# Performance work log

Measured on AMD Instinct MI355X. Metric: run time of the kernel, lower is better.

## Reference

```python
import jax, jax.numpy as jnp
import numpy as np

N_CLI, N_AGG, E, D, L = 100000, 1000, 1600000, 128, 3


def setup_inputs() -> dict:
    key = jax.random.key(0)
    ks = jax.random.split(key, 16)
    inp = {
        'x_clients': jax.random.normal(ks[0], (N_CLI, D), jnp.float32),
        'x_agg': jax.random.normal(ks[1], (N_AGG, D), jnp.float32),
        'c2a_src': jax.random.randint(ks[2], (E,), 0, N_CLI, jnp.int32),
        'c2a_dst': jax.random.randint(ks[3], (E,), 0, N_AGG, jnp.int32),
        'a2c_src': jax.random.randint(ks[4], (E,), 0, N_AGG, jnp.int32),
        'a2c_dst': jax.random.randint(ks[5], (E,), 0, N_CLI, jnp.int32),
    }
    s = 1.0 / np.sqrt(D)
    # stacked per-layer SAGE params for each edge type: W_l (on aggregated msg), W_r (on dst), b
    inp['Wl_c2a'] = jax.random.uniform(ks[6], (L, D, D), jnp.float32, -s, s)
    inp['Wr_c2a'] = jax.random.uniform(ks[7], (L, D, D), jnp.float32, -s, s)
    inp['b_c2a'] = jax.random.uniform(ks[8], (L, D), jnp.float32, -s, s)
    inp['Wl_a2c'] = jax.random.uniform(ks[9], (L, D, D), jnp.float32, -s, s)
    inp['Wr_a2c'] = jax.random.uniform(ks[10], (L, D, D), jnp.float32, -s, s)
    inp['b_a2c'] = jax.random.uniform(ks[11], (L, D), jnp.float32, -s, s)
    inp['W_lin'] = jax.random.uniform(ks[12], (D, 1), jnp.float32, -s, s)
    inp['b_lin'] = jax.random.uniform(ks[13], (1,), jnp.float32, -s, s)
    return inp


def _sage(x_src, x_dst, src, dst, Wl, Wr, b, n_dst):
    # mean aggregation of gathered source features onto dst nodes
    msg = x_src[src]                                        # [E, D]
    summed = jax.ops.segment_sum(msg, dst, num_segments=n_dst)
    cnt = jax.ops.segment_sum(jnp.ones((src.shape[0], 1), x_src.dtype), dst, num_segments=n_dst)
    mean = summed / jnp.maximum(cnt, 1.0)
    return mean @ Wl + x_dst @ Wr + b


def _leaky(x):
    return jnp.where(x >= 0, x, 0.1 * x)


def reference(x_clients, x_agg, c2a_src, c2a_dst, a2c_src, a2c_dst,
              Wl_c2a, Wr_c2a, b_c2a, Wl_a2c, Wr_a2c, b_a2c, W_lin, b_lin):
    xc, xa = x_clients, x_agg
    for l in range(L):
        new_a = _sage(xc, xa, c2a_src, c2a_dst, Wl_c2a[l], Wr_c2a[l], b_c2a[l], N_AGG)
        new_c = _sage(xa, xc, a2c_src, a2c_dst, Wl_a2c[l], Wr_a2c[l], b_a2c[l], N_CLI)
        xa, xc = _leaky(new_a), _leaky(new_c)
    return (xc @ W_lin + b_lin).squeeze(1)
```

## Files before the change

### kernel.cpp

```cpp
#include <hip/hip_runtime.h>

#define D      128
#define NCLI   100000
#define NAGG   1000
#define NLAYER 3
#define NBKT   782
#define NRNG   8
#define NBIN   (NAGG * NRNG)
#define RMAGIC 343598u
#define NHIST  512
#define NCVTX  (NCLI * D / 4 / 256)
#define NCVTW  ((NLAYER * D * D + 255) / 256)
#define NROWT  (NCLI / 32)
#define CAP_E  1536

typedef short bf16x8 __attribute__((ext_vector_type(8)));
typedef float f32x16 __attribute__((ext_vector_type(16)));

static __device__ __forceinline__ float leaky(float x) { return x >= 0.f ? x : 0.1f * x; }

static __device__ __forceinline__ unsigned bf16_rn(float f) {
    unsigned u = __float_as_uint(f);
    return (u + 0x7fffu + ((u >> 16) & 1u)) >> 16;
}
static __device__ __forceinline__ float bf_val(unsigned h) { return __uint_as_float(h << 16); }
static __device__ __forceinline__ unsigned pack_bf2(float lo, float hi) {
    return bf16_rn(lo) | (bf16_rn(hi) << 16);
}
static __device__ __forceinline__ float bf_lo(unsigned v) { return __uint_as_float(v << 16); }
static __device__ __forceinline__ float bf_hi(unsigned v) { return __uint_as_float(v & 0xffff0000u); }

__global__ __launch_bounds__(256) void prep(const int* __restrict__ c2a_src,
                                            const int* __restrict__ c2a_dst,
                                            const int* __restrict__ a2c_dst, int E,
                                            int* __restrict__ cnt_ar, int* __restrict__ bcnt,
                                            const float4* __restrict__ X4,
                                            uint2* __restrict__ xhi, uint2* __restrict__ xlo,
                                            const float* __restrict__ W,
                                            unsigned short* __restrict__ Wt) {
    __shared__ int h[NBIN + NBKT];
    int bid = blockIdx.x;
    if (bid < NHIST) {
        for (int i = threadIdx.x; i < NBIN + NBKT; i += 256) h[i] = 0;
        __syncthreads();
        int stride = NHIST * 256;
        for (int e = bid * 256 + threadIdx.x; e < E; e += stride) {
            int s = c2a_src[e];
            int bin = c2a_dst[e] * NRNG + (int)__umulhi((unsigned)s, RMAGIC);
            atomicAdd(&h[bin], 1);
            atomicAdd(&h[NBIN + (a2c_dst[e] >> 7)], 1);
        }
        __syncthreads();
        for (int i = threadIdx.x; i < NBIN; i += 256)
            if (h[i]) atomicAdd(&cnt_ar[i], h[i]);
        for (int i = threadIdx.x; i < NBKT; i += 256)
            if (h[NBIN + i]) atomicAdd(&bcnt[i], h[NBIN + i]);
    } else if (bid < NHIST + NCVTX) {
        int t = (bid - NHIST) * 256 + threadIdx.x;
        float4 f = X4[t];
        unsigned h0 = bf16_rn(f.x), h1 = bf16_rn(f.y), h2 = bf16_rn(f.z), h3 = bf16_rn(f.w);
        xhi[t] = make_uint2(h0 | (h1 << 16), h2 | (h3 << 16));
        xlo[t] = make_uint2(pack_bf2(f.x - bf_val(h0), f.y - bf_val(h1)),
                            pack_bf2(f.z - bf_val(h2), f.w - bf_val(h3)));
    } else {
        int idx = (bid - NHIST - NCVTX) * 256 + threadIdx.x;
        if (idx >= NLAYER * D * D) return;
        int layer = idx >> 14, rem = idx & (D * D - 1);
        int k = rem >> 7, n = rem & 127;
        float w = W[layer * D * D + k * D + n];
        unsigned hh = bf16_rn(w);
        unsigned short* base = Wt + layer * 2 * D * D;
        base[n * D + k] = (unsigned short)hh;
        base[D * D + n * D + k] = (unsigned short)bf16_rn(w - bf_val(hh));
    }
}

__global__ void scan_both(const int* __restrict__ cnt_ar, int* __restrict__ rp_ar,
                          int* __restrict__ cur_ar, const int* __restrict__ bcnt,
                          int* __restrict__ brp, int* __restrict__ bcur) {
    __shared__ int sh[1024];
    int t = threadIdx.x;
    if (blockIdx.x == 0) {
        int v[8];
        int s = 0;
#pragma unroll
        for (int j = 0; j < 8; j++) {
            int idx = t * 8 + j;
            v[j] = (idx < NBIN) ? cnt_ar[idx] : 0;
            s += v[j];
        }
        sh[t] = s;
        __syncthreads();
        for (int off = 1; off < 1024; off <<= 1) {
            int x = (t >= off) ? sh[t - off] : 0;
            __syncthreads();
            sh[t] += x;
            __syncthreads();
        }
        int run = sh[t] - s;
#pragma unroll
        for (int j = 0; j < 8; j++) {
            int idx = t * 8 + j;
            if (idx < NBIN) {
                rp_ar[idx] = run;
                cur_ar[idx] = run;
            }
            run += v[j];
        }
        if (t == 1023) rp_ar[NBIN] = sh[1023];
    } else {
        int v = (t < NBKT) ? bcnt[t] : 0;
        sh[t] = v;
        __syncthreads();
        for (int off = 1; off < 1024; off <<= 1) {
            int x = (t >= off) ? sh[t - off] : 0;
            __syncthreads();
            sh[t] += x;
            __syncthreads();
        }
        if (t == 0) { brp[0] = 0; bcur[0] = 0; }
        if (t < NBKT) {
            brp[t + 1] = sh[t];
            if (t + 1 < NBKT) bcur[t + 1] = sh[t];
        }
    }
}

__global__ __launch_bounds__(1024) void scatter_both(const int* __restrict__ c2a_src,
                                                     const int* __restrict__ c2a_dst,
                                                     const int* __restrict__ a2c_src,
                                                     const int* __restrict__ a2c_dst, int E,
                                                     int* __restrict__ cur_ar,
                                                     int* __restrict__ col_c2a,
                                                     int* __restrict__ bcur,
                                                     int* __restrict__ sorted1) {
    __shared__ int sbuf[2 * NBIN];
    int tid = threadIdx.x;
    if (blockIdx.x < 256) {
        int* h = sbuf;
        int* base = sbuf + NBIN;
        int chunk = (E + 255) / 256;
        int e0 = blockIdx.x * chunk;
        int e1 = min(E, e0 + chunk);
        for (int i = tid; i < NBIN; i += 1024) h[i] = 0;
        __syncthreads();
        for (int e = e0 + tid; e < e1; e += 1024) {
            int s = c2a_src[e];
            atomicAdd(&h[c2a_dst[e] * NRNG + (int)__umulhi((unsigned)s, RMAGIC)], 1);
        }
        __syncthreads();
        for (int i = tid; i < NBIN; i += 1024) {
            int c = h[i];
            base[i] = c ? atomicAdd(&cur_ar[i], c) : 0;
        }
        __syncthreads();
        for (int e = e0 + tid; e < e1; e += 1024) {
            int s = c2a_src[e];
            int bin = c2a_dst[e] * NRNG + (int)__umulhi((unsigned)s, RMAGIC);
            int pos = atomicAdd(&base[bin], 1);
            col_c2a[pos] = s;
        }
    } else {
        int* h = sbuf;
        int* base = sbuf + NBKT;
        int bid = blockIdx.x - 256;
        int chunk = (E + 255) / 256;
        int e0 = bid * chunk;
        int e1 = min(E, e0 + chunk);
        for (int i = tid; i < NBKT; i += 1024) h[i] = 0;
        __syncthreads();
        for (int e = e0 + tid; e < e1; e += 1024) atomicAdd(&h[a2c_dst[e] >> 7], 1);
        __syncthreads();
        for (int i = tid; i < NBKT; i += 1024) {
            int c = h[i];
            base[i] = c ? atomicAdd(&bcur[i], c) : 0;
        }
        __syncthreads();
        for (int e = e0 + tid; e < e1; e += 1024) {
            int d = a2c_dst[e];
            int pos = atomicAdd(&base[d >> 7], 1);
            sorted1[pos] = ((d & 127) << 10) | a2c_src[e];
        }
    }
}

__global__ __launch_bounds__(512) void bucket_csr(const int* __restrict__ brp,
                                                  const int* __restrict__ sorted1,
                                                  int* __restrict__ rp_c,
                                                  int* __restrict__ col) {
    __shared__ int h[128], cur[128];
    int b = blockIdx.x, tid = threadIdx.x;
    if (tid < 128) h[tid] = 0;
    __syncthreads();
    int beg = brp[b], end = brp[b + 1];
    for (int e = beg + tid; e < end; e += 512) atomicAdd(&h[sorted1[e] >> 10], 1);
    __syncthreads();
    if (tid < 128) cur[tid] = h[tid];
    __syncthreads();
    for (int off = 1; off < 128; off <<= 1) {
        int x = 0;
        if (tid < 128 && tid >= off) x = cur[tid - off];
        __syncthreads();
        if (tid < 128) cur[tid] += x;
        __syncthreads();
    }
    if (tid < 128) {
        int start = beg + cur[tid] - h[tid];
        int c = b * 128 + tid;
        if (c < NCLI) rp_c[c] = start;
        cur[tid] = start;
    }
    if (b == NBKT - 1 && tid == 0) rp_c[NCLI] = end;
    __syncthreads();
    for (int e = beg + tid; e < end; e += 512) {
        int p = sorted1[e];
        int pos = atomicAdd(&cur[p >> 10], 1);
        col[pos] = p & 1023;
    }
}


__global__ __launch_bounds__(512) void gather_mean(const unsigned* __restrict__ tbl,
                                                   const int* __restrict__ rp_ar,
                                                   const int* __restrict__ col,
                                                   float* __restrict__ psum) {
    __shared__ float part[4][8][D];
    int quad = blockIdx.x >> 3, r = blockIdx.x & 7;
    int tid = threadIdx.x;
    int a = tid >> 7;
    int sub = (tid >> 4) & 7;
    int sl = tid & 15;
    const uint4* tbl4 = (const uint4*)tbl;
    int agg = quad * 4 + a;
    int bin = agg * NRNG + r;
    int beg = rp_ar[bin], end = rp_ar[bin + 1];
    float f0 = 0, f1 = 0, f2 = 0, f3 = 0, f4 = 0, f5 = 0, f6 = 0, f7 = 0;
    int e = beg + sub;
    for (; e + 8 < end; e += 16) {
        int s0 = col[e];
        int s1 = col[e + 8];
        uint4 v0 = tbl4[(s0 << 4) + sl];
        uint4 v1 = tbl4[(s1 << 4) + sl];
        f0 += bf_lo(v0.x); f1 += bf_hi(v0.x); f2 += bf_lo(v0.y); f3 += bf_hi(v0.y);
        f4 += bf_lo(v0.z); f5 += bf_hi(v0.z); f6 += bf_lo(v0.w); f7 += bf_hi(v0.w);
        f0 += bf_lo(v1.x); f1 += bf_hi(v1.x); f2 += bf_lo(v1.y); f3 += bf_hi(v1.y);
        f4 += bf_lo(v1.z); f5 += bf_hi(v1.z); f6 += bf_lo(v1.w); f7 += bf_hi(v1.w);
    }
    if (e < end) {
        int s0 = col[e];
        uint4 v0 = tbl4[(s0 << 4) + sl];
        f0 += bf_lo(v0.x); f1 += bf_hi(v0.x); f2 += bf_lo(v0.y); f3 += bf_hi(v0.y);
        f4 += bf_lo(v0.z); f5 += bf_hi(v0.z); f6 += bf_lo(v0.w); f7 += bf_hi(v0.w);
    }
    float* pr = &part[a][sub][sl * 8];
    pr[0] = f0; pr[1] = f1; pr[2] = f2; pr[3] = f3;
    pr[4] = f4; pr[5] = f5; pr[6] = f6; pr[7] = f7;
    __syncthreads();
    int c = tid & 127;
    float s = 0.f;
#pragma unroll
    for (int g = 0; g < 8; g++) s += part[a][g][c];
    psum[((size_t)agg * NRNG + r) * D + c] = s;
}

__global__ __launch_bounds__(128) void combine_agg(const float* __restrict__ psum,
                                                   const int* __restrict__ rp_ar,
                                                   const float* xa_old,
                                                   const float* __restrict__ Wl_a2c,
                                                   const float* __restrict__ Wl_c2a,
                                                   const float* __restrict__ Wr_c2a,
                                                   const float* __restrict__ b_c2a,
                                                   unsigned short* __restrict__ ya_bf,
                                                   float* xa_out) {
    __shared__ float mr[D], xr[D];
    int i = blockIdx.x, j = threadIdx.x;
    const float* pr = psum + (size_t)i * NRNG * D + j;
    float s = 0.f;
#pragma unroll
    for (int r = 0; r < NRNG; r++) s += pr[r * D];
    int deg = rp_ar[i * NRNG + NRNG] - rp_ar[i * NRNG];
    mr[j] = s / fmaxf((float)deg, 1.f);
    xr[j] = xa_old[i * D + j];
    __syncthreads();
    float accy = 0.f, accn = b_c2a[j];
#pragma unroll 4
    for (int k = 0; k < D; k++) {
        accy += xr[k] * Wl_a2c[k * D + j];
        accn += mr[k] * Wl_c2a[k * D + j] + xr[k] * Wr_c2a[k * D + j];
    }
    ya_bf[i * D + j] = (unsigned short)bf16_rn(accy);
    xa_out[i * D + j] = leaky(accn);
}

#define ACC8(vv) do { \
    s0 += bf_lo(vv.x); s1 += bf_hi(vv.x); s2 += bf_lo(vv.y); s3 += bf_hi(vv.y); \
    s4 += bf_lo(vv.z); s5 += bf_hi(vv.z); s6 += bf_lo(vv.w); s7 += bf_hi(vv.w); } while (0)

#define GBLOCK(SRC) do { \
    int r0 = (SRC)[0], r1 = (SRC)[1], r2 = (SRC)[2], r3 = (SRC)[3]; \
    int r4 = (SRC)[4], r5 = (SRC)[5], r6 = (SRC)[6], r7 = (SRC)[7]; \
    uint4 v0 = ya4[(r0 << 4) + q]; uint4 v1 = ya4[(r1 << 4) + q]; \
    uint4 v2 = ya4[(r2 << 4) + q]; uint4 v3 = ya4[(r3 << 4) + q]; \
    uint4 v4 = ya4[(r4 << 4) + q]; uint4 v5 = ya4[(r5 << 4) + q]; \
    uint4 v6 = ya4[(r6 << 4) + q]; uint4 v7 = ya4[(r7 << 4) + q]; \
    ACC8(v0); ACC8(v1); ACC8(v2); ACC8(v3); \
    ACC8(v4); ACC8(v5); ACC8(v6); ACC8(v7); } while (0)

#define GTAIL(SRC) do { \
    int rr = (SRC)[0]; \
    uint4 v = ya4[(rr << 4) + q]; \
    ACC8(v); } while (0)

template <int LAST>
__global__ __launch_bounds__(256) void gemm_agg(const unsigned short* __restrict__ Ahi,
                                                const unsigned short* __restrict__ Alo,
                                                const unsigned short* __restrict__ Wt,
                                                const float* __restrict__ bias,
                                                const unsigned* __restrict__ ya,
                                                const int* __restrict__ rowptr,
                                                const int* __restrict__ col,
                                                unsigned* __restrict__ xhi,
                                                unsigned* __restrict__ xlo,
                                                const float* __restrict__ Wlin,
                                                const float* __restrict__ blin,
                                                float* __restrict__ out, int E) {
    __shared__ float smem[32][D];
    __shared__ int lcol[CAP_E];
    int tid = threadIdx.x;
    int wave = tid >> 6, lane = tid & 63;
    int cl = lane & 31, kh = lane >> 5;
    int n0 = wave * 32;
    int m0 = blockIdx.x * 32;
    int blkBeg = rowptr[m0], blkEnd = rowptr[m0 + 32];
    int nE = blkEnd - blkBeg;
    bool inlds = (nE <= CAP_E);
    int pv[6];
#pragma unroll
    for (int k = 0; k < 6; k++) pv[k] = col[min(blkBeg + tid + k * 256, E - 1)];
    const unsigned short* Wlo_ = Wt + D * D;
    const unsigned short* wbh = Wt + (size_t)(n0 + cl) * D + kh * 8;
    const unsigned short* wbl = Wlo_ + (size_t)(n0 + cl) * D + kh * 8;
    bf16x8 bhi[8], blo[8];
#pragma unroll
    for (int kc = 0; kc < 8; kc++) {
        bhi[kc] = *(const bf16x8*)(wbh + kc * 16);
        blo[kc] = *(const bf16x8*)(wbl + kc * 16);
    }
    float bv = bias[n0 + cl];
    {
        const unsigned short* ar = Ahi + (size_t)(m0 + cl) * D + kh * 8;
        const unsigned short* al = Alo + (size_t)(m0 + cl) * D + kh * 8;
        bf16x8 ahi[8], alo[8];
#pragma unroll
        for (int kc = 0; kc < 8; kc++) {
            ahi[kc] = *(const bf16x8*)(ar + kc * 16);
            alo[kc] = *(const bf16x8*)(al + kc * 16);
        }
        if (inlds) {
#pragma unroll
            for (int k = 0; k < 6; k++) lcol[tid + k * 256] = pv[k];
        }
        f32x16 acc;
#pragma unroll
        for (int q = 0; q < 16; q++) acc[q] = bv;
#pragma unroll
        for (int kc = 0; kc < 8; kc++) {
            acc = __builtin_amdgcn_mfma_f32_32x32x16_bf16(ahi[kc], bhi[kc], acc, 0, 0, 0);
            acc = __builtin_amdgcn_mfma_f32_32x32x16_bf16(alo[kc], bhi[kc], acc, 0, 0, 0);
            acc = __builtin_amdgcn_mfma_f32_32x32x16_bf16(ahi[kc], blo[kc], acc, 0, 0, 0);
        }
#pragma unroll
        for (int reg = 0; reg < 16; reg++) {
            int row = (reg & 3) + 8 * (reg >> 2) + 4 * kh;
            smem[row][n0 + cl] = acc[reg];
        }
    }
    __syncthreads();
    const uint4* ya4 = (const uint4*)ya;
    int g = lane >> 4, q = lane & 15;
#pragma unroll
    for (int pass = 0; pass < 2; pass++) {
        int c_local = wave * 8 + pass * 4 + g;
        int gid = m0 + c_local;
        int beg = rowptr[gid], end = rowptr[gid + 1];
        int len = end - beg;
        float s0 = 0, s1 = 0, s2 = 0, s3 = 0, s4 = 0, s5 = 0, s6 = 0, s7 = 0;
        if (inlds) {
            const int* src = lcol + (beg - blkBeg);
            int j = 0;
            for (; j + 8 <= len; j += 8) GBLOCK(src + j);
            for (; j < len; j++) GTAIL(src + j);
        } else {
            const int* src = col + beg;
            int j = 0;
            for (; j + 8 <= len; j += 8) GBLOCK(src + j);
            for (; j < len; j++) GTAIL(src + j);
        }
        float inv = 1.f / fmaxf((float)len, 1.f);
        float4 y0 = *(const float4*)&smem[c_local][8 * q];
        float4 y1 = *(const float4*)&smem[c_local][8 * q + 4];
        float r0 = leaky(y0.x + s0 * inv);
        float r1 = leaky(y0.y + s1 * inv);
        float r2 = leaky(y0.z + s2 * inv);
        float r3 = leaky(y0.w + s3 * inv);
        float r4 = leaky(y1.x + s4 * inv);
        float r5 = leaky(y1.y + s5 * inv);
        float r6 = leaky(y1.z + s6 * inv);
        float r7 = leaky(y1.w + s7 * inv);
        if (LAST) {
            float4 w0 = *(const float4*)&Wlin[8 * q];
            float4 w1 = *(const float4*)&Wlin[8 * q + 4];
            float v = r0 * w0.x + r1 * w0.y + r2 * w0.z + r3 * w0.w +
                      r4 * w1.x + r5 * w1.y + r6 * w1.z + r7 * w1.w;
#pragma unroll
            for (int off = 8; off > 0; off >>= 1) v += __shfl_down(v, off, 16);
            if (q == 0) out[gid] = v + blin[0];
        } else {
            unsigned h0 = bf16_rn(r0), h1 = bf16_rn(r1), h2 = bf16_rn(r2), h3 = bf16_rn(r3);
            unsigned h4 = bf16_rn(r4), h5 = bf16_rn(r5), h6 = bf16_rn(r6), h7 = bf16_rn(r7);
            uint4 hi, lo;
            hi.x = h0 | (h1 << 16); hi.y = h2 | (h3 << 16);
            hi.z = h4 | (h5 << 16); hi.w = h6 | (h7 << 16);
            lo.x = pack_bf2(r0 - bf_val(h0), r1 - bf_val(h1));
            lo.y = pack_bf2(r2 - bf_val(h2), r3 - bf_val(h3));
            lo.z = pack_bf2(r4 - bf_val(h4), r5 - bf_val(h5));
            lo.w = pack_bf2(r6 - bf_val(h6), r7 - bf_val(h7));
            ((uint4*)xhi)[(gid << 4) + q] = hi;
            ((uint4*)xlo)[(gid << 4) + q] = lo;
        }
    }
}

extern "C" void kernel_launch(void* const* d_in, const int* in_sizes, int n_in,
                              void* d_out, int out_size, void* d_ws, size_t ws_size,
                              hipStream_t stream) {
    const float* x_clients = (const float*)d_in[0];
    const float* x_agg     = (const float*)d_in[1];
    const int*   c2a_src   = (const int*)d_in[2];
    const int*   c2a_dst   = (const int*)d_in[3];
    const int*   a2c_src   = (const int*)d_in[4];
    const int*   a2c_dst   = (const int*)d_in[5];
    const float* Wl_c2a    = (const float*)d_in[6];
    const float* Wr_c2a    = (const float*)d_in[7];
    const float* b_c2a     = (const float*)d_in[8];
    const float* Wl_a2c    = (const float*)d_in[9];
    const float* Wr_a2c    = (const float*)d_in[10];
    const float* b_a2c     = (const float*)d_in[11];
    const float* W_lin     = (const float*)d_in[12];
    const float* b_lin     = (const float*)d_in[13];
    float* out = (float*)d_out;
    const int E = in_sizes[2];

    char* p = (char*)d_ws;
    auto alloc = [&](size_t bytes) {
        char* r = p;
        p += (bytes + 255) & ~(size_t)255;
        return r;
    };
    float*    Yb    = (float*)alloc(sizeof(float) * NCLI * D);
    unsigned* xc_hi = (unsigned*)alloc(sizeof(unsigned) * NCLI * 64);
    unsigned* xc_lo = (unsigned*)alloc(sizeof(unsigned) * NCLI * 64);
    float*    xa    = (float*)alloc(sizeof(float) * NAGG * D);
    unsigned short* ya_bf = (unsigned short*)alloc(sizeof(unsigned short) * NAGG * D);
    unsigned short* Wt = (unsigned short*)alloc(sizeof(unsigned short) * NLAYER * 2 * D * D);
    float* psum  = (float*)alloc(sizeof(float) * NAGG * NRNG * D);
    int* cnt_ar = (int*)alloc(sizeof(int) * (NBIN + NBKT));
    int* bcnt  = cnt_ar + NBIN;
    int* rp_ar = (int*)alloc(sizeof(int) * (NBIN + 1));
    int* cur_ar = (int*)alloc(sizeof(int) * NBIN);
    int* brp   = (int*)alloc(sizeof(int) * (NBKT + 1));
    int* bcur  = (int*)alloc(sizeof(int) * NBKT);
    int* rp_c  = (int*)alloc(sizeof(int) * (NCLI + 1));
    int* col_c2a = (int*)alloc(sizeof(int) * E);
    int* col_a2c = (int*)alloc(sizeof(int) * E);
    int* sorted1 = (int*)Yb;

    hipMemsetAsync(cnt_ar, 0, sizeof(int) * (NBIN + NBKT), stream);

    prep<<<NHIST + NCVTX + NCVTW, 256, 0, stream>>>(c2a_src, c2a_dst, a2c_dst, E, cnt_ar, bcnt,
                                                    (const float4*)x_clients,
                                                    (uint2*)xc_hi, (uint2*)xc_lo,
                                                    Wr_a2c, Wt);
    scan_both<<<2, 1024, 0, stream>>>(cnt_ar, rp_ar, cur_ar, bcnt, brp, bcur);
    scatter_both<<<512, 1024, 0, stream>>>(c2a_src, c2a_dst, a2c_src, a2c_dst, E,
                                           cur_ar, col_c2a, bcur, sorted1);
    bucket_csr<<<NBKT, 512, 0, stream>>>(brp, sorted1, rp_c, col_a2c);

    const float* xa_old = x_agg;
    for (int l = 0; l < NLAYER; l++) {
        gather_mean<<<(NAGG / 4) * NRNG, 512, 0, stream>>>(xc_hi, rp_ar, col_c2a, psum);
        combine_agg<<<NAGG, 128, 0, stream>>>(psum, rp_ar, xa_old,
                                              Wl_a2c + l * D * D, Wl_c2a + l * D * D,
                                              Wr_c2a + l * D * D, b_c2a + l * D, ya_bf, xa);
        if (l < NLAYER - 1) {
            gemm_agg<0><<<NROWT, 256, 0, stream>>>(
                (const unsigned short*)xc_hi, (const unsigned short*)xc_lo,
                Wt + l * 2 * D * D, b_a2c + l * D, (const unsigned*)ya_bf, rp_c, col_a2c,
                xc_hi, xc_lo, nullptr, nullptr, nullptr, E);
        } else {
            gemm_agg<1><<<NROWT, 256, 0, stream>>>(
                (const unsigned short*)xc_hi, (const unsigned short*)xc_lo,
                Wt + l * 2 * D * D, b_a2c + l * D, (const unsigned*)ya_bf, rp_c, col_a2c,
                nullptr, nullptr, W_lin, b_lin, out, E);
        }
        xa_old = xa;
    }
}
```

Baseline: 615.3 us.

## Use two-pass coarse-then-refine bucket sort for both edge CSR builds

New measurement: 598.0 us. -2.8%, faster.

```diff
diff --git a/kernel.cpp b/kernel.cpp
--- a/kernel.cpp
+++ b/kernel.cpp
@@ -4,7 +4,8 @@
 #define NCLI   100000
 #define NAGG   1000
 #define NLAYER 3
-#define NBKT   782
+#define NBKT   98
+#define NC2A   63
 #define NRNG   8
 #define NBIN   (NAGG * NRNG)
 #define RMAGIC 343598u
@@ -48,7 +49,7 @@
             int s = c2a_src[e];
             int bin = c2a_dst[e] * NRNG + (int)__umulhi((unsigned)s, RMAGIC);
             atomicAdd(&h[bin], 1);
-            atomicAdd(&h[NBIN + (a2c_dst[e] >> 7)], 1);
+            atomicAdd(&h[NBIN + (a2c_dst[e] >> 10)], 1);
         }
         __syncthreads();
         for (int i = threadIdx.x; i < NBIN; i += 256)
@@ -76,8 +77,9 @@
 }
 
 __global__ void scan_both(const int* __restrict__ cnt_ar, int* __restrict__ rp_ar,
-                          int* __restrict__ cur_ar, const int* __restrict__ bcnt,
-                          int* __restrict__ brp, int* __restrict__ bcur) {
+                          const int* __restrict__ bcnt,
+                          int* __restrict__ brp, int* __restrict__ bcur,
+                          int* __restrict__ ccur) {
     __shared__ int sh[1024];
     int t = threadIdx.x;
     if (blockIdx.x == 0) {
@@ -101,13 +103,12 @@
 #pragma unroll
         for (int j = 0; j < 8; j++) {
             int idx = t * 8 + j;
-            if (idx < NBIN) {
-                rp_ar[idx] = run;
-                cur_ar[idx] = run;
-            }
+            if (idx < NBIN) rp_ar[idx] = run;
             run += v[j];
         }
         if (t == 1023) rp_ar[NBIN] = sh[1023];
+        __syncthreads();
+        if (t < NC2A) ccur[t] = rp_ar[t * 128];
     } else {
         int v = (t < NBKT) ? bcnt[t] : 0;
         sh[t] = v;
@@ -126,50 +127,47 @@
     }
 }
 
-__global__ __launch_bounds__(1024) void scatter_both(const int* __restrict__ c2a_src,
-                                                     const int* __restrict__ c2a_dst,
-                                                     const int* __restrict__ a2c_src,
-                                                     const int* __restrict__ a2c_dst, int E,
-                                                     int* __restrict__ cur_ar,
-                                                     int* __restrict__ col_c2a,
-                                                     int* __restrict__ bcur,
-                                                     int* __restrict__ sorted1) {
-    __shared__ int sbuf[2 * NBIN];
+__global__ __launch_bounds__(1024) void scatter_coarse(const int* __restrict__ c2a_src,
+                                                       const int* __restrict__ c2a_dst,
+                                                       const int* __restrict__ a2c_src,
+                                                       const int* __restrict__ a2c_dst, int E,
+                                                       int* __restrict__ ccur,
+                                                       int* __restrict__ tmp1,
+                                                       int* __restrict__ bcur,
+                                                       int* __restrict__ tmp2) {
+    __shared__ int h[NBKT], base[NBKT];
     int tid = threadIdx.x;
     if (blockIdx.x < 256) {
-        int* h = sbuf;
-        int* base = sbuf + NBIN;
         int chunk = (E + 255) / 256;
         int e0 = blockIdx.x * chunk;
         int e1 = min(E, e0 + chunk);
-        for (int i = tid; i < NBIN; i += 1024) h[i] = 0;
-        __syncthreads();
-        for (int e = e0 + tid; e < e1; e += 1024) {
-            int s = c2a_src[e];
-            atomicAdd(&h[c2a_dst[e] * NRNG + (int)__umulhi((unsigned)s, RMAGIC)], 1);
-        }
-        __syncthreads();
-        for (int i = tid; i < NBIN; i += 1024) {
-            int c = h[i];
-            base[i] = c ? atomicAdd(&cur_ar[i], c) : 0;
-        }
+        for (int i = tid; i < NC2A; i += 1024) h[i] = 0;
         __syncthreads();
         for (int e = e0 + tid; e < e1; e += 1024) {
             int s = c2a_src[e];
             int bin = c2a_dst[e] * NRNG + (int)__umulhi((unsigned)s, RMAGIC);
-            int pos = atomicAdd(&base[bin], 1);
-            col_c2a[pos] = s;
+            atomicAdd(&h[bin >> 7], 1);
+        }
+        __syncthreads();
+        for (int i = tid; i < NC2A; i += 1024) {
+            int c = h[i];
+            base[i] = c ? atomicAdd(&ccur[i], c) : 0;
+        }
+        __syncthreads();
+        for (int e = e0 + tid; e < e1; e += 1024) {
+            int s = c2a_src[e];
+            int bin = c2a_dst[e] * NRNG + (int)__umulhi((unsigned)s, RMAGIC);
+            int pos = atomicAdd(&base[bin >> 7], 1);
+            tmp1[pos] = (bin << 17) | s;
         }
     } else {
-        int* h = sbuf;
-        int* base = sbuf + NBKT;
         int bid = blockIdx.x - 256;
         int chunk = (E + 255) / 256;
         int e0 = bid * chunk;
         int e1 = min(E, e0 + chunk);
         for (int i = tid; i < NBKT; i += 1024) h[i] = 0;
         __syncthreads();
-        for (int e = e0 + tid; e < e1; e += 1024) atomicAdd(&h[a2c_dst[e] >> 7], 1);
+        for (int e = e0 + tid; e < e1; e += 1024) atomicAdd(&h[a2c_dst[e] >> 10], 1);
         __syncthreads();
         for (int i = tid; i < NBKT; i += 1024) {
             int c = h[i];
@@ -178,44 +176,61 @@
         __syncthreads();
         for (int e = e0 + tid; e < e1; e += 1024) {
             int d = a2c_dst[e];
-            int pos = atomicAdd(&base[d >> 7], 1);
-            sorted1[pos] = ((d & 127) << 10) | a2c_src[e];
-        }
-    }
-}
-
-__global__ __launch_bounds__(512) void bucket_csr(const int* __restrict__ brp,
-                                                  const int* __restrict__ sorted1,
-                                                  int* __restrict__ rp_c,
-                                                  int* __restrict__ col) {
-    __shared__ int h[128], cur[128];
-    int b = blockIdx.x, tid = threadIdx.x;
-    if (tid < 128) h[tid] = 0;
-    __syncthreads();
-    int beg = brp[b], end = brp[b + 1];
-    for (int e = beg + tid; e < end; e += 512) atomicAdd(&h[sorted1[e] >> 10], 1);
-    __syncthreads();
-    if (tid < 128) cur[tid] = h[tid];
-    __syncthreads();
-    for (int off = 1; off < 128; off <<= 1) {
-        int x = 0;
-        if (tid < 128 && tid >= off) x = cur[tid - off];
-        __syncthreads();
-        if (tid < 128) cur[tid] += x;
-        __syncthreads();
-    }
-    if (tid < 128) {
-        int start = beg + cur[tid] - h[tid];
-        int c = b * 128 + tid;
+            int pos = atomicAdd(&base[d >> 10], 1);
+            tmp2[pos] = ((d & 1023) << 10) | a2c_src[e];
+        }
+    }
+}
+
+__global__ __launch_bounds__(1024) void refine(const int* __restrict__ rp_ar,
+                                               const int* __restrict__ tmp1,
+                                               int* __restrict__ col_c2a,
+                                               const int* __restrict__ brp,
+                                               const int* __restrict__ tmp2,
+                                               int* __restrict__ rp_c,
+                                               int* __restrict__ col_a2c) {
+    int tid = threadIdx.x;
+    if (blockIdx.x < NC2A) {
+        __shared__ int lcur[128];
+        int c = blockIdx.x;
+        int b0 = c * 128;
+        int nb = min(128, NBIN - b0);
+        if (tid < nb) lcur[tid] = rp_ar[b0 + tid];
+        int beg = rp_ar[b0];
+        int end = rp_ar[min(b0 + 128, NBIN)];
+        __syncthreads();
+        for (int e = beg + tid; e < end; e += 1024) {
+            int v = tmp1[e];
+            int pos = atomicAdd(&lcur[(v >> 17) - b0], 1);
+            col_c2a[pos] = v & 0x1FFFF;
+        }
+    } else {
+        __shared__ int h2[1024], cur2[1024];
+        int b = blockIdx.x - NC2A;
+        int beg = brp[b], end = brp[b + 1];
+        h2[tid] = 0;
+        __syncthreads();
+        for (int e = beg + tid; e < end; e += 1024) atomicAdd(&h2[tmp2[e] >> 10], 1);
+        __syncthreads();
+        cur2[tid] = h2[tid];
+        __syncthreads();
+        for (int off = 1; off < 1024; off <<= 1) {
+            int x = (tid >= off) ? cur2[tid - off] : 0;
+            __syncthreads();
+            cur2[tid] += x;
+            __syncthreads();
+        }
+        int start = beg + cur2[tid] - h2[tid];
+        int c = b * 1024 + tid;
         if (c < NCLI) rp_c[c] = start;
-        cur[tid] = start;
-    }
-    if (b == NBKT - 1 && tid == 0) rp_c[NCLI] = end;
-    __syncthreads();
-    for (int e = beg + tid; e < end; e += 512) {
-        int p = sorted1[e];
-        int pos = atomicAdd(&cur[p >> 10], 1);
-        col[pos] = p & 1023;
+        cur2[tid] = start;
+        if (b == NBKT - 1 && tid == 0) rp_c[NCLI] = end;
+        __syncthreads();
+        for (int e = beg + tid; e < end; e += 1024) {
+            int p = tmp2[e];
+            int pos = atomicAdd(&cur2[p >> 10], 1);
+            col_a2c[pos] = p & 1023;
+        }
     }
 }
 
@@ -467,13 +482,14 @@
     int* cnt_ar = (int*)alloc(sizeof(int) * (NBIN + NBKT));
     int* bcnt  = cnt_ar + NBIN;
     int* rp_ar = (int*)alloc(sizeof(int) * (NBIN + 1));
-    int* cur_ar = (int*)alloc(sizeof(int) * NBIN);
     int* brp   = (int*)alloc(sizeof(int) * (NBKT + 1));
     int* bcur  = (int*)alloc(sizeof(int) * NBKT);
+    int* ccur  = (int*)alloc(sizeof(int) * NC2A);
     int* rp_c  = (int*)alloc(sizeof(int) * (NCLI + 1));
     int* col_c2a = (int*)alloc(sizeof(int) * E);
     int* col_a2c = (int*)alloc(sizeof(int) * E);
-    int* sorted1 = (int*)Yb;
+    int* tmp1 = (int*)Yb;
+    int* tmp2 = tmp1 + E;
 
     hipMemsetAsync(cnt_ar, 0, sizeof(int) * (NBIN + NBKT), stream);
 
@@ -481,10 +497,10 @@
                                                     (const float4*)x_clients,
                                                     (uint2*)xc_hi, (uint2*)xc_lo,
                                                     Wr_a2c, Wt);
-    scan_both<<<2, 1024, 0, stream>>>(cnt_ar, rp_ar, cur_ar, bcnt, brp, bcur);
-    scatter_both<<<512, 1024, 0, stream>>>(c2a_src, c2a_dst, a2c_src, a2c_dst, E,
-                                           cur_ar, col_c2a, bcur, sorted1);
-    bucket_csr<<<NBKT, 512, 0, stream>>>(brp, sorted1, rp_c, col_a2c);
+    scan_both<<<2, 1024, 0, stream>>>(cnt_ar, rp_ar, bcnt, brp, bcur, ccur);
+    scatter_coarse<<<512, 1024, 0, stream>>>(c2a_src, c2a_dst, a2c_src, a2c_dst, E,
+                                             ccur, tmp1, bcur, tmp2);
+    refine<<<NC2A + NBKT, 1024, 0, stream>>>(rp_ar, tmp1, col_c2a, brp, tmp2, rp_c, col_a2c);
 
     const float* xa_old = x_agg;
     for (int l = 0; l < NLAYER; l++) {
```
